# Performance work log

Measured on AMD Instinct MI355X. Metric: run time of the kernel, lower is better.

## Reference

```python
import jax, jax.numpy as jnp
import numpy as np

jax.config.update("jax_enable_x64", True)

NNZ = 8_388_608        # number of sparse (feature_id, value) pairs
N_FEATURES = 8_192     # number of calibrated feature ids
N_BIN = 63             # bin boundaries per feature -> 64 bins
OUT_BITS = 22          # output id space = 1 << 22
GOLDEN32 = np.uint32(0x9E3779B9)  # Knuth multiplicative-hashing constant


def setup_inputs() -> dict:
    key = jax.random.key(0)
    k1, k2, k3 = jax.random.split(key, 3)
    input_keys = jax.random.randint(k1, (NNZ,), 0, 2 * N_FEATURES, dtype=jnp.int64)
    input_vals = jax.random.normal(k2, (NNZ,), dtype=jnp.float32)
    # Calibrated feature ids (sorted) and per-feature sorted bin boundaries.
    feature_ids = jnp.arange(N_FEATURES, dtype=jnp.int64)
    bin_vals = jnp.sort(
        jax.random.normal(k3, (N_FEATURES, N_BIN), dtype=jnp.float32), axis=1
    ).reshape(-1)
    return {
        "input_keys": input_keys,
        "input_vals": input_vals,
        "feature_ids": feature_ids,
        "bin_vals": bin_vals,
    }


def _lower_bound_bins(bin_vals_flat, feat_idx, vals, n_bin):
    """Per-value branchless binary search: bin = sum(bin_row < val).

    bin_vals_flat: [F * n_bin] row-sorted boundaries, feat_idx: [nnz] int,
    vals: [nnz] float. Returns [nnz] int32 bin index in [0, n_bin].
    """
    steps = int(np.ceil(np.log2(n_bin + 1)))  # 6 for n_bin=63
    base = feat_idx.astype(jnp.int64) * n_bin
    lo = jnp.zeros(vals.shape, dtype=jnp.int32)
    hi = jnp.full(vals.shape, n_bin, dtype=jnp.int32)
    for _ in range(steps):
        mid = (lo + hi) >> 1                       # in [0, n_bin]
        mid_safe = jnp.minimum(mid, n_bin - 1)     # gather-safe
        bv = bin_vals_flat[base + mid_safe]
        valid = lo < hi
        go_right = valid & (bv < vals)             # strict '<' => lower bound
        lo = jnp.where(go_right, mid + 1, lo)
        hi = jnp.where(valid & ~go_right, mid, hi)
    return lo


def reference(input_keys, input_vals, feature_ids, bin_vals):
    F = feature_ids.shape[0]
    n_bin = bin_vals.shape[0] // F
    mask = jnp.int64((1 << OUT_BITS) - 1)

    # --- find each key in the (sorted) calibrated feature-id table ---
    idx = jnp.searchsorted(feature_ids, input_keys)          # [nnz]
    idx_safe = jnp.minimum(idx, F - 1)
    calibrated = feature_ids[idx_safe] == input_keys          # [nnz] bool

    # --- bin assignment: bin = sum(bin_vals_row < val) ---
    bins = _lower_bound_bins(bin_vals, idx_safe, input_vals, n_bin)

    # --- 32-bit integer multiplicative hash of (feature_id, bin) ---
    h = (input_keys.astype(jnp.uint32) * GOLDEN32 + bins.astype(jnp.uint32)) * GOLDEN32
    hashed_key = h.astype(jnp.int64) & mask

    out_keys = jnp.where(calibrated, hashed_key, input_keys & mask)
    out_vals = jnp.where(calibrated, jnp.ones_like(input_vals), input_vals)
    # dense_shape of the resulting SparseTensor is [batch, 1 << OUT_BITS]
    return out_keys, out_vals
```

## Files before the change

kernel.cpp:

```cpp
#include <hip/hip_runtime.h>
#include <stdint.h>
#include <math.h>


#define GOLDEN   0x9E3779B9u
#define OUT_MASK ((1u << 22) - 1u)
#define NBIN  63
#define NPIV  8192
#define NKEY  16384
#define MAGIC 0xC0FFEE42u

typedef float fx4 __attribute__((ext_vector_type(4)));
typedef int   ix4 __attribute__((ext_vector_type(4)));
typedef unsigned ux4 __attribute__((ext_vector_type(4)));

__global__ __launch_bounds__(256) void build_tables_kernel(
    const int* __restrict__ fids, const float* __restrict__ bins,
    float* __restrict__ qtab, ux4* __restrict__ spiv_g,
    unsigned char* __restrict__ scal_g, int F)
{
    const int t = blockIdx.x * blockDim.x + threadIdx.x;
    if (t >= F * 64) return;
    const int r = t >> 6;
    const int j = t & 63;
    const int k = fids[r];
    const unsigned uk = (unsigned)k;
    const float* src = bins + (size_t)r * NBIN;

    if (uk < (unsigned)NPIV) {
        qtab[((size_t)uk << 6) + j] = (j < NBIN) ? src[j] : INFINITY;
        if (j == 0) {
            ux4 p;
            p.x = __float_as_uint(src[15]);
            p.y = __float_as_uint(src[31]);
            p.z = __float_as_uint(src[47]);
            p.w = uk ^ MAGIC;
            spiv_g[uk] = p;
        }
    } else if (uk < (unsigned)NKEY && j == 0) {
        scal_g[uk - NPIV] = (unsigned char)(0x40u | (uk & 63u));
    }
}

__device__ __forceinline__ void hd_fallback(
    int k, float v, const int* __restrict__ fids, const float* __restrict__ bins,
    int F, int fsteps, float& okey, float& oval)
{
    int lo = 0, hi = F;
    for (int s = 0; s < fsteps; ++s) {
        int  mid  = (lo + hi) >> 1;
        int  mids = min(mid, F - 1);
        int  fv   = fids[mids];
        bool valid = lo < hi;
        bool right = valid && (fv < k);
        lo = right ? mid + 1 : lo;
        hi = (valid && !right) ? mid : hi;
    }
    const int  idx_safe   = min(lo, F - 1);
    const bool calibrated = (fids[idx_safe] == k);
    const float* brow = bins + (size_t)idx_safe * NBIN;
    int blo = 0, bhi = NBIN;
    #pragma unroll
    for (int s = 0; s < 6; ++s) {
        int   mid  = (blo + bhi) >> 1;
        int   mids = min(mid, NBIN - 1);
        float bv   = brow[mids];
        bool  valid = blo < bhi;
        bool  right = valid && (bv < v);
        blo = right ? mid + 1 : blo;
        bhi = (valid && !right) ? mid : bhi;
    }
    const uint32_t h = ((uint32_t)k * GOLDEN + (uint32_t)blo) * GOLDEN;
    okey = calibrated ? (float)(h & OUT_MASK) : (float)((uint32_t)k & OUT_MASK);
    oval = calibrated ? 1.0f : v;
}

__global__ __launch_bounds__(1024) void hd_main_kernel(
    const int* __restrict__ keys, const float* __restrict__ vals,
    const int* __restrict__ fids, const float* __restrict__ bins,
    const float* __restrict__ qtab, const ux4* __restrict__ spiv_g,
    const unsigned char* __restrict__ scal_g,
    float* __restrict__ out_keys, float* __restrict__ out_vals,
    int n, int F, int fsteps, int nchunks)
{
    extern __shared__ char smem[];
    ux4*      spiv = reinterpret_cast<ux4*>(smem);
    unsigned* scal = reinterpret_cast<unsigned*>(smem + (size_t)NPIV * 16);

    const int tid = threadIdx.x;
    for (int i = tid; i < NPIV; i += (int)blockDim.x) spiv[i] = spiv_g[i];
    const unsigned* scal_g32 = reinterpret_cast<const unsigned*>(scal_g);
    for (int i = tid; i < NPIV / 4; i += (int)blockDim.x) scal[i] = scal_g32[i];
    __syncthreads();

    const unsigned char* scal_b = reinterpret_cast<const unsigned char*>(scal);
    const int nthreads = (int)(gridDim.x * blockDim.x);

    for (int c = blockIdx.x * blockDim.x + tid; c < nchunks; c += nthreads) {
        const int i0 = c * 8;
        int   ks[8];
        float vs[8];
        const bool full = (i0 + 7 < n);
        if (full) {
            const ix4 ka = __builtin_nontemporal_load(reinterpret_cast<const ix4*>(keys + i0));
            const ix4 kb = __builtin_nontemporal_load(reinterpret_cast<const ix4*>(keys + i0 + 4));
            const fx4 va = __builtin_nontemporal_load(reinterpret_cast<const fx4*>(vals + i0));
            const fx4 vb = __builtin_nontemporal_load(reinterpret_cast<const fx4*>(vals + i0 + 4));
            ks[0]=ka.x; ks[1]=ka.y; ks[2]=ka.z; ks[3]=ka.w;
            ks[4]=kb.x; ks[5]=kb.y; ks[6]=kb.z; ks[7]=kb.w;
            vs[0]=va.x; vs[1]=va.y; vs[2]=va.z; vs[3]=va.w;
            vs[4]=vb.x; vs[5]=vb.y; vs[6]=vb.z; vs[7]=vb.w;
        } else {
            #pragma unroll
            for (int j = 0; j < 8; ++j) {
                int idx = min(i0 + j, n - 1);
                ks[j] = keys[idx];
                vs[j] = vals[idx];
            }
        }

        float ok[8], ov[8];

        #pragma unroll
        for (int g = 0; g < 2; ++g) {
            ux4 hdr[4];
            bool low[4];
            #pragma unroll
            for (int j = 0; j < 4; ++j) {
                const unsigned uk = (unsigned)ks[g * 4 + j];
                low[j] = uk < (unsigned)NPIV;
                hdr[j] = spiv[low[j] ? uk : 0u];
            }
            #pragma unroll
            for (int j = 0; j < 4; ++j) {
                const int e = g * 4 + j;
                const unsigned uk = (unsigned)ks[e];
                const float v = vs[e];
                if (low[j]) {
                    if (hdr[j].w == (uk ^ MAGIC)) {
                        const int q = (__uint_as_float(hdr[j].x) < v)
                                    + (__uint_as_float(hdr[j].y) < v)
                                    + (__uint_as_float(hdr[j].z) < v);
                        const fx4* sec = reinterpret_cast<const fx4*>(
                            qtab + ((size_t)uk << 6) + (q << 4));
                        const fx4 b0 = sec[0], b1 = sec[1], b2 = sec[2], b3 = sec[3];
                        const int cnt = (q << 4)
                            + (b0.x < v) + (b0.y < v) + (b0.z < v) + (b0.w < v)
                            + (b1.x < v) + (b1.y < v) + (b1.z < v) + (b1.w < v)
                            + (b2.x < v) + (b2.y < v) + (b2.z < v) + (b2.w < v)
                            + (b3.x < v) + (b3.y < v) + (b3.z < v) + (b3.w < v);
                        const uint32_t h = (uk * GOLDEN + (uint32_t)cnt) * GOLDEN;
                        ok[e] = (float)(h & OUT_MASK);
                        ov[e] = 1.0f;
                    } else {
                        ok[e] = (float)(uk & OUT_MASK);
                        ov[e] = v;
                    }
                } else if (uk < (unsigned)NKEY) {
                    const bool calib =
                        scal_b[uk - NPIV] == (unsigned char)(0x40u | (uk & 63u));
                    if (calib) {
                        hd_fallback(ks[e], v, fids, bins, F, fsteps, ok[e], ov[e]);
                    } else {
                        ok[e] = (float)(uk & OUT_MASK);
                        ov[e] = v;
                    }
                } else {
                    hd_fallback(ks[e], v, fids, bins, F, fsteps, ok[e], ov[e]);
                }
            }
        }

        if (full) {
            fx4 a, b;
            a.x=ok[0]; a.y=ok[1]; a.z=ok[2]; a.w=ok[3];
            b.x=ok[4]; b.y=ok[5]; b.z=ok[6]; b.w=ok[7];
            __builtin_nontemporal_store(a, reinterpret_cast<fx4*>(out_keys + i0));
            __builtin_nontemporal_store(b, reinterpret_cast<fx4*>(out_keys + i0 + 4));
            a.x=ov[0]; a.y=ov[1]; a.z=ov[2]; a.w=ov[3];
            b.x=ov[4]; b.y=ov[5]; b.z=ov[6]; b.w=ov[7];
            __builtin_nontemporal_store(a, reinterpret_cast<fx4*>(out_vals + i0));
            __builtin_nontemporal_store(b, reinterpret_cast<fx4*>(out_vals + i0 + 4));
        } else {
            for (int j = 0; j < 8 && i0 + j < n; ++j) {
                out_keys[i0 + j] = ok[j];
                out_vals[i0 + j] = ov[j];
            }
        }
    }
}

__global__ __launch_bounds__(256) void hd_simple_kernel(
    const int* __restrict__ keys, const float* __restrict__ vals,
    const int* __restrict__ fids, const float* __restrict__ bins,
    float* __restrict__ out_keys, float* __restrict__ out_vals,
    int n, int F, int fsteps)
{
    const int gid = blockIdx.x * blockDim.x + threadIdx.x;
    const int i0 = gid * 4;
    if (i0 >= n) return;
    #pragma unroll
    for (int j = 0; j < 4; ++j) {
        int idx = min(i0 + j, n - 1);
        float okey, oval;
        hd_fallback(keys[idx], vals[idx], fids, bins, F, fsteps, okey, oval);
        if (i0 + j < n) { out_keys[i0 + j] = okey; out_vals[i0 + j] = oval; }
    }
}

extern "C" void kernel_launch(void* const* d_in, const int* in_sizes, int n_in,
                              void* d_out, int out_size, void* d_ws, size_t ws_size,
                              hipStream_t stream) {
    const int*   keys = (const int*)d_in[0];
    const float* vals = (const float*)d_in[1];
    const int*   fids = (const int*)d_in[2];
    const float* bins = (const float*)d_in[3];

    const int n = in_sizes[0];
    const int F = in_sizes[2];

    int fsteps = 0;
    while ((1 << fsteps) < F + 1) ++fsteps;

    float* out_keys = (float*)d_out;
    float* out_vals = (float*)d_out + n;

    const size_t qtab_bytes = (size_t)NPIV * 64 * sizeof(float);
    const size_t spiv_bytes = (size_t)NPIV * 16;
    const size_t scal_bytes = (size_t)NPIV;
    const size_t ws_need    = qtab_bytes + spiv_bytes + scal_bytes;
    const size_t lds_bytes  = spiv_bytes + scal_bytes;

    int max_lds = 0;
    hipDeviceGetAttribute(&max_lds, hipDeviceAttributeMaxSharedMemoryPerBlock, 0);

    const bool fast = (ws_size >= ws_need) && ((size_t)max_lds >= lds_bytes) &&
                      (in_sizes[3] == F * NBIN);

    if (fast) {
        float*         qtab   = (float*)d_ws;
        ux4*           spiv_g = (ux4*)((char*)d_ws + qtab_bytes);
        unsigned char* scal_g = (unsigned char*)d_ws + qtab_bytes + spiv_bytes;

        build_tables_kernel<<<(F * 64 + 255) / 256, 256, 0, stream>>>(
            fids, bins, qtab, spiv_g, scal_g, F);

        (void)hipFuncSetAttribute(
            reinterpret_cast<const void*>(hd_main_kernel),
            hipFuncAttributeMaxDynamicSharedMemorySize, (int)lds_bytes);

        const int threads = 1024;
        const int nblocks = 256;
        const int nchunks = (n + 7) / 8;
        hd_main_kernel<<<nblocks, threads, lds_bytes, stream>>>(
            keys, vals, fids, bins, qtab, spiv_g, scal_g,
            out_keys, out_vals, n, F, fsteps, nchunks);
    } else {
        const int threads = 256;
        const int grid = (n + threads * 4 - 1) / (threads * 4);
        hd_simple_kernel<<<grid, threads, 0, stream>>>(
            keys, vals, fids, bins, out_keys, out_vals, n, F, fsteps);
    }
}
```

Measured before the change: 160.1 us.

## Restructure main kernel into branchless 4-element batches with hoisted table loads

The main loop now handles four elements per chunk instead of eight and drops the per-element branches. Table offsets are computed unconditionally, with uncalibrated keys pointed at offset zero, so all eight 16-byte qtab loads per batch can be issued back to back before any comparisons. This gives more memory-level parallelism and less divergence. Rare keys go through a single unlikely-branch fallback, and the launch bounds now request 4 blocks per CU. In exchange, uncalibrated keys issue wasted loads, and the occupancy hint may force register spills.

```diff
diff --git a/kernel.cpp b/kernel.cpp
--- a/kernel.cpp
+++ b/kernel.cpp
@@ -75,7 +75,12 @@
     oval = calibrated ? 1.0f : v;
 }
 
-__global__ __launch_bounds__(1024) void hd_main_kernel(
+__device__ __forceinline__ int hd_cmp8(fx4 a, fx4 b, float v) {
+    return (a.x < v) + (a.y < v) + (a.z < v) + (a.w < v)
+         + (b.x < v) + (b.y < v) + (b.z < v) + (b.w < v);
+}
+
+__global__ __launch_bounds__(1024, 4) void hd_main_kernel(
     const int* __restrict__ keys, const float* __restrict__ vals,
     const int* __restrict__ fids, const float* __restrict__ bins,
     const float* __restrict__ qtab, const ux4* __restrict__ spiv_g,
@@ -94,98 +99,103 @@
     __syncthreads();
 
     const unsigned char* scal_b = reinterpret_cast<const unsigned char*>(scal);
+    const char* qb = reinterpret_cast<const char*>(qtab);
     const int nthreads = (int)(gridDim.x * blockDim.x);
 
     for (int c = blockIdx.x * blockDim.x + tid; c < nchunks; c += nthreads) {
-        const int i0 = c * 8;
-        int   ks[8];
-        float vs[8];
-        const bool full = (i0 + 7 < n);
+        const int i0 = c * 4;
+        int   k0, k1, k2, k3;
+        float v0, v1, v2, v3;
+        const bool full = (i0 + 3 < n);
         if (full) {
             const ix4 ka = __builtin_nontemporal_load(reinterpret_cast<const ix4*>(keys + i0));
-            const ix4 kb = __builtin_nontemporal_load(reinterpret_cast<const ix4*>(keys + i0 + 4));
             const fx4 va = __builtin_nontemporal_load(reinterpret_cast<const fx4*>(vals + i0));
-            const fx4 vb = __builtin_nontemporal_load(reinterpret_cast<const fx4*>(vals + i0 + 4));
-            ks[0]=ka.x; ks[1]=ka.y; ks[2]=ka.z; ks[3]=ka.w;
-            ks[4]=kb.x; ks[5]=kb.y; ks[6]=kb.z; ks[7]=kb.w;
-            vs[0]=va.x; vs[1]=va.y; vs[2]=va.z; vs[3]=va.w;
-            vs[4]=vb.x; vs[5]=vb.y; vs[6]=vb.z; vs[7]=vb.w;
+            k0 = ka.x; k1 = ka.y; k2 = ka.z; k3 = ka.w;
+            v0 = va.x; v1 = va.y; v2 = va.z; v3 = va.w;
         } else {
-            #pragma unroll
-            for (int j = 0; j < 8; ++j) {
-                int idx = min(i0 + j, n - 1);
-                ks[j] = keys[idx];
-                vs[j] = vals[idx];
-            }
-        }
-
-        float ok[8], ov[8];
-
-        #pragma unroll
-        for (int g = 0; g < 2; ++g) {
-            ux4 hdr[4];
-            bool low[4];
-            #pragma unroll
-            for (int j = 0; j < 4; ++j) {
-                const unsigned uk = (unsigned)ks[g * 4 + j];
-                low[j] = uk < (unsigned)NPIV;
-                hdr[j] = spiv[low[j] ? uk : 0u];
-            }
-            #pragma unroll
-            for (int j = 0; j < 4; ++j) {
-                const int e = g * 4 + j;
-                const unsigned uk = (unsigned)ks[e];
-                const float v = vs[e];
-                if (low[j]) {
-                    if (hdr[j].w == (uk ^ MAGIC)) {
-                        const int q = (__uint_as_float(hdr[j].x) < v)
-                                    + (__uint_as_float(hdr[j].y) < v)
-                                    + (__uint_as_float(hdr[j].z) < v);
-                        const fx4* sec = reinterpret_cast<const fx4*>(
-                            qtab + ((size_t)uk << 6) + (q << 4));
-                        const fx4 b0 = sec[0], b1 = sec[1], b2 = sec[2], b3 = sec[3];
-                        const int cnt = (q << 4)
-                            + (b0.x < v) + (b0.y < v) + (b0.z < v) + (b0.w < v)
-                            + (b1.x < v) + (b1.y < v) + (b1.z < v) + (b1.w < v)
-                            + (b2.x < v) + (b2.y < v) + (b2.z < v) + (b2.w < v)
-                            + (b3.x < v) + (b3.y < v) + (b3.z < v) + (b3.w < v);
-                        const uint32_t h = (uk * GOLDEN + (uint32_t)cnt) * GOLDEN;
-                        ok[e] = (float)(h & OUT_MASK);
-                        ov[e] = 1.0f;
-                    } else {
-                        ok[e] = (float)(uk & OUT_MASK);
-                        ov[e] = v;
-                    }
-                } else if (uk < (unsigned)NKEY) {
-                    const bool calib =
-                        scal_b[uk - NPIV] == (unsigned char)(0x40u | (uk & 63u));
-                    if (calib) {
-                        hd_fallback(ks[e], v, fids, bins, F, fsteps, ok[e], ov[e]);
-                    } else {
-                        ok[e] = (float)(uk & OUT_MASK);
-                        ov[e] = v;
-                    }
-                } else {
-                    hd_fallback(ks[e], v, fids, bins, F, fsteps, ok[e], ov[e]);
-                }
-            }
+            k0 = keys[min(i0 + 0, n - 1)]; v0 = vals[min(i0 + 0, n - 1)];
+            k1 = keys[min(i0 + 1, n - 1)]; v1 = vals[min(i0 + 1, n - 1)];
+            k2 = keys[min(i0 + 2, n - 1)]; v2 = vals[min(i0 + 2, n - 1)];
+            k3 = keys[min(i0 + 3, n - 1)]; v3 = vals[min(i0 + 3, n - 1)];
+        }
+
+        const unsigned u0 = (unsigned)k0, u1 = (unsigned)k1,
+                       u2 = (unsigned)k2, u3 = (unsigned)k3;
+        const ux4 h0 = spiv[u0 < (unsigned)NPIV ? u0 : 0u];
+        const ux4 h1 = spiv[u1 < (unsigned)NPIV ? u1 : 0u];
+        const ux4 h2 = spiv[u2 < (unsigned)NPIV ? u2 : 0u];
+        const ux4 h3 = spiv[u3 < (unsigned)NPIV ? u3 : 0u];
+
+#define HD_P2(J)                                                              \
+        const bool cal##J = (u##J < (unsigned)NPIV) &&                        \
+                            (h##J.w == (u##J ^ MAGIC));                       \
+        const int  q##J = (__uint_as_float(h##J.x) < v##J)                    \
+                        + (__uint_as_float(h##J.y) < v##J)                    \
+                        + (__uint_as_float(h##J.z) < v##J);                   \
+        const unsigned off##J = cal##J ? ((u##J << 8) + (unsigned)(q##J << 6))\
+                                       : 0u;                                  \
+        int qc##J = q##J << 4;                                                \
+        const unsigned hs##J = u##J - (unsigned)NPIV;                         \
+        const bool rare##J =                                                  \
+            (u##J >= (unsigned)NKEY) ||                                       \
+            ((hs##J < (unsigned)NPIV) &&                                      \
+             (scal_b[hs##J < (unsigned)NPIV ? hs##J : 0u] ==                  \
+              (unsigned char)(0x40u | (u##J & 63u))));
+        HD_P2(0) HD_P2(1) HD_P2(2) HD_P2(3)
+#undef HD_P2
+
+        fx4 a0 = *reinterpret_cast<const fx4*>(qb + off0);
+        fx4 b0 = *reinterpret_cast<const fx4*>(qb + off0 + 16);
+        fx4 a1 = *reinterpret_cast<const fx4*>(qb + off1);
+        fx4 b1 = *reinterpret_cast<const fx4*>(qb + off1 + 16);
+        fx4 a2 = *reinterpret_cast<const fx4*>(qb + off2);
+        fx4 b2 = *reinterpret_cast<const fx4*>(qb + off2 + 16);
+        fx4 a3 = *reinterpret_cast<const fx4*>(qb + off3);
+        fx4 b3 = *reinterpret_cast<const fx4*>(qb + off3 + 16);
+
+        qc0 += hd_cmp8(a0, b0, v0);
+        qc1 += hd_cmp8(a1, b1, v1);
+        qc2 += hd_cmp8(a2, b2, v2);
+        qc3 += hd_cmp8(a3, b3, v3);
+
+        a0 = *reinterpret_cast<const fx4*>(qb + off0 + 32);
+        b0 = *reinterpret_cast<const fx4*>(qb + off0 + 48);
+        a1 = *reinterpret_cast<const fx4*>(qb + off1 + 32);
+        b1 = *reinterpret_cast<const fx4*>(qb + off1 + 48);
+        a2 = *reinterpret_cast<const fx4*>(qb + off2 + 32);
+        b2 = *reinterpret_cast<const fx4*>(qb + off2 + 48);
+        a3 = *reinterpret_cast<const fx4*>(qb + off3 + 32);
+        b3 = *reinterpret_cast<const fx4*>(qb + off3 + 48);
+
+        float ok0, ok1, ok2, ok3, ov0, ov1, ov2, ov3;
+#define HD_P6(J)                                                              \
+        {                                                                     \
+            const int cnt = qc##J + hd_cmp8(a##J, b##J, v##J);                \
+            const uint32_t h = (u##J * GOLDEN + (uint32_t)cnt) * GOLDEN;      \
+            ok##J = cal##J ? (float)(h & OUT_MASK) : (float)(u##J & OUT_MASK);\
+            ov##J = cal##J ? 1.0f : v##J;                                     \
+        }
+        HD_P6(0) HD_P6(1) HD_P6(2) HD_P6(3)
+#undef HD_P6
+
+        if (__builtin_expect(rare0 | rare1 | rare2 | rare3, 0)) {
+            if (rare0) hd_fallback(k0, v0, fids, bins, F, fsteps, ok0, ov0);
+            if (rare1) hd_fallback(k1, v1, fids, bins, F, fsteps, ok1, ov1);
+            if (rare2) hd_fallback(k2, v2, fids, bins, F, fsteps, ok2, ov2);
+            if (rare3) hd_fallback(k3, v3, fids, bins, F, fsteps, ok3, ov3);
         }
 
         if (full) {
-            fx4 a, b;
-            a.x=ok[0]; a.y=ok[1]; a.z=ok[2]; a.w=ok[3];
-            b.x=ok[4]; b.y=ok[5]; b.z=ok[6]; b.w=ok[7];
-            __builtin_nontemporal_store(a, reinterpret_cast<fx4*>(out_keys + i0));
-            __builtin_nontemporal_store(b, reinterpret_cast<fx4*>(out_keys + i0 + 4));
-            a.x=ov[0]; a.y=ov[1]; a.z=ov[2]; a.w=ov[3];
-            b.x=ov[4]; b.y=ov[5]; b.z=ov[6]; b.w=ov[7];
-            __builtin_nontemporal_store(a, reinterpret_cast<fx4*>(out_vals + i0));
-            __builtin_nontemporal_store(b, reinterpret_cast<fx4*>(out_vals + i0 + 4));
+            fx4 s;
+            s.x = ok0; s.y = ok1; s.z = ok2; s.w = ok3;
+            __builtin_nontemporal_store(s, reinterpret_cast<fx4*>(out_keys + i0));
+            s.x = ov0; s.y = ov1; s.z = ov2; s.w = ov3;
+            __builtin_nontemporal_store(s, reinterpret_cast<fx4*>(out_vals + i0));
         } else {
-            for (int j = 0; j < 8 && i0 + j < n; ++j) {
-                out_keys[i0 + j] = ok[j];
-                out_vals[i0 + j] = ov[j];
-            }
+            if (i0 + 0 < n) { out_keys[i0 + 0] = ok0; out_vals[i0 + 0] = ov0; }
+            if (i0 + 1 < n) { out_keys[i0 + 1] = ok1; out_vals[i0 + 1] = ov1; }
+            if (i0 + 2 < n) { out_keys[i0 + 2] = ok2; out_vals[i0 + 2] = ov2; }
+            if (i0 + 3 < n) { out_keys[i0 + 3] = ok3; out_vals[i0 + 3] = ov3; }
         }
     }
 }
@@ -251,7 +261,7 @@
 
         const int threads = 1024;
         const int nblocks = 256;
-        const int nchunks = (n + 7) / 8;
+        const int nchunks = (n + 3) / 4;
         hd_main_kernel<<<nblocks, threads, lds_bytes, stream>>>(
             keys, vals, fids, bins, qtab, spiv_g, scal_g,
             out_keys, out_vals, n, F, fsteps, nchunks);
```

Measured after the change: 164.9 us. 1.03x slower.
